# Performance work log

Hardware: AMD Instinct MI355X
Metric: run time of the kernel (lower is better)

Reference implementation:

```python
import jax, jax.numpy as jnp
import numpy as np

N_NODES = 100000
SELF_LOOP_W = 2.0  # improved=True in GCNConv -> A + 2I


def gcn_conv(x, src, dst, ew, W, b):
    """PyG GCNConv(improved=True): D^-1/2 (A + 2I) D^-1/2 X W + b.

    src/dst: edge endpoints, messages flow src -> dst (source_to_target).
    """
    n = x.shape[0]
    # degree after adding self loops with weight 2.0
    deg = jnp.zeros((n,), dtype=x.dtype).at[dst].add(ew) + SELF_LOOP_W
    dinv = jax.lax.rsqrt(deg)
    norm = dinv[src] * ew * dinv[dst]                      # [E]
    h = x @ W                                              # [N, out]
    agg = jax.ops.segment_sum(norm[:, None] * h[src], dst, num_segments=n)
    self_term = (SELF_LOOP_W * dinv * dinv)[:, None] * h   # self-loop edges
    return agg + self_term + b


def setup_inputs() -> dict:
    key = jax.random.key(0)
    ks = jax.random.split(key, 10)
    F_IN, H1, H2, C = 128, 128, 64, 5
    E = 1600000
    x = jax.random.normal(ks[0], (N_NODES, F_IN), dtype=jnp.float32)
    edge_index = jax.random.randint(ks[1], (2, E), 0, N_NODES, dtype=jnp.int64)
    edge_weight = jax.random.uniform(ks[2], (E,), dtype=jnp.float32)

    def glorot(k, shape):
        lim = float(np.sqrt(6.0 / (shape[0] + shape[1])))
        return jax.random.uniform(k, shape, jnp.float32, -lim, lim)

    return {
        "x": x,
        "edge_index": edge_index,
        "edge_weight": edge_weight,
        "W1": glorot(ks[3], (F_IN, H1)), "b1": jnp.zeros((H1,), jnp.float32),
        "W2": glorot(ks[4], (H1, H2)),  "b2": jnp.zeros((H2,), jnp.float32),
        "Wc": glorot(ks[5], (H2, C)),   "bc": jnp.zeros((C,), jnp.float32),
    }


def reference(x, edge_index, edge_weight, W1, b1, W2, b2, Wc, bc):
    src, dst = edge_index[0], edge_index[1]
    # conv1 + relu (dropout is identity in eval mode)
    h = jax.nn.relu(gcn_conv(x, src, dst, edge_weight, W1, b1))
    # conv2 + relu
    h = jax.nn.relu(gcn_conv(h, src, dst, edge_weight, W2, b2))
    # classifier head + log_softmax over classes
    logits = gcn_conv(h, src, dst, edge_weight, Wc, bc)
    return jax.nn.log_softmax(logits, axis=1)
```

## Files before the change

### kernel.cpp

```cpp
#include <hip/hip_runtime.h>
#include <hip/hip_bf16.h>

constexpr int TPB = 256;

static inline int cdiv(long long a, long long b) { return (int)((a + b - 1) / b); }

typedef __attribute__((ext_vector_type(8))) short bf16x8;
typedef __attribute__((ext_vector_type(4))) float f32x4;

__device__ inline unsigned short f2bf(float f) {
    __hip_bfloat16 h = __float2bfloat16(f);
    unsigned short u;
    __builtin_memcpy(&u, &h, 2);
    return u;
}

__device__ inline float bflo(unsigned u) { return __uint_as_float(u << 16); }
__device__ inline float bfhi(unsigned u) { return __uint_as_float(u & 0xffff0000u); }

__device__ inline unsigned relu_pk(unsigned w) {
    unsigned lo = (w & 0x8000u) ? 0u : (w & 0xFFFFu);
    unsigned hi = (w & 0x80000000u) ? 0u : (w & 0xFFFF0000u);
    return lo | hi;
}

constexpr int P1_CH   = 4096;
constexpr int MAXBINS = 512;
constexpr int BINCAP  = 4608;

__device__ __forceinline__ void part_body(const int* __restrict__ src,
                                          const int* __restrict__ dst,
                                          const float* __restrict__ ew,
                                          int* __restrict__ bincnt,
                                          int2* __restrict__ pbuf, int E, int nbins,
                                          int* h, int bid) {
    for (int t = threadIdx.x; t < nbins; t += TPB) h[t] = 0;
    __syncthreads();
    const int lo = bid * P1_CH;
    const int hi = min(lo + P1_CH, E);
    for (int e = lo + threadIdx.x; e < hi; e += TPB)
        atomicAdd(&h[dst[e] >> 8], 1);
    __syncthreads();
    for (int t = threadIdx.x; t < nbins; t += TPB) {
        int c = h[t];
        h[t] = (c > 0) ? atomicAdd(&bincnt[t], c) : 0;
    }
    __syncthreads();
    for (int e = lo + threadIdx.x; e < hi; e += TPB) {
        int d = dst[e];
        int bin = d >> 8;
        int idx = atomicAdd(&h[bin], 1);
        if (idx < BINCAP)
            pbuf[(size_t)bin * BINCAP + idx] =
                make_int2((src[e] & 0x1FFFF) | ((d & 255) << 24), __float_as_int(ew[e]));
    }
}

template<int CAP>
__global__ __launch_bounds__(TPB) void k_bucket(const int2* __restrict__ pbuf,
                                                const int* __restrict__ bincnt,
                                                int2* __restrict__ pairs,
                                                int* __restrict__ cnt,
                                                float* __restrict__ dinv, int n) {
    __shared__ int   lcnt[TPB];
    __shared__ float ldeg[TPB];
    const int tid = threadIdx.x;
    lcnt[tid] = 0; ldeg[tid] = 0.f;
    __syncthreads();
    const int bin = blockIdx.x;
    const int m = min(bincnt[bin], BINCAP);
    const int2* pb = pbuf + (size_t)bin * BINCAP;
    for (int i = tid; i < m; i += TPB) {
        int2 pe = pb[i];
        int dlo = (pe.x >> 24) & 255;
        int s   = pe.x & 0x1FFFF;
        int pos = atomicAdd(&lcnt[dlo], 1);
        if (pos < CAP)
            pairs[(size_t)(bin * 256 + dlo) * CAP + pos] = make_int2(s, pe.y);
        atomicAdd(&ldeg[dlo], __int_as_float(pe.y));
    }
    __syncthreads();
    int node = bin * 256 + tid;
    if (node < n) {
        cnt[node]  = min(lcnt[tid], CAP);
        dinv[node] = rsqrtf(ldeg[tid] + 2.0f);
    }
}

template<int CAP>
__global__ void k_bucket_scatter(const int* __restrict__ src, const int* __restrict__ dst,
                                 const float* __restrict__ ew, int* __restrict__ cnt,
                                 int2* __restrict__ pairs, int E) {
    int e = blockIdx.x * TPB + threadIdx.x;
    if (e >= E) return;
    int d = dst[e];
    int pos = atomicAdd(&cnt[d], 1);
    if (pos < CAP)
        pairs[(size_t)d * CAP + pos] = make_int2(src[e], __float_as_int(ew[e]));
}

template<int CAP>
__global__ void k_deg(const int2* __restrict__ pairs, const int* __restrict__ cnt,
                      float* __restrict__ dinv, int n) {
    int node = blockIdx.x * (TPB / 64) + (threadIdx.x >> 6);
    if (node >= n) return;
    int lane = threadIdx.x & 63;
    int m = min(cnt[node], CAP);
    float v = 0.f;
    if (lane < m) v = __int_as_float(pairs[(size_t)node * CAP + lane].y);
#pragma unroll
    for (int d = 1; d < 64; d <<= 1) v += __shfl_xor(v, d);
    if (lane == 0) dinv[node] = rsqrtf(v + 2.0f);
}

template<int CAP>
__global__ void k_normw(int2* __restrict__ pairs, const int* __restrict__ cnt,
                        const float* __restrict__ dinv, int n) {
    int lane = threadIdx.x & 63;
    int g = lane >> 4, o = lane & 15;
    int wid = blockIdx.x * (TPB / 64) + (threadIdx.x >> 6);
    int node = wid * 4 + g;
    if (node >= n) return;
    int m = min(cnt[node], CAP);
    float dd = dinv[node];
    int2* pr = pairs + (size_t)node * CAP;
    for (int j = o; j < m; j += 16) {
        int2 p = pr[j];
        pr[j].y = __float_as_int(dinv[p.x] * __int_as_float(p.y) * dd);
    }
}

__global__ void k_prepw(const float* __restrict__ W1, const float* __restrict__ W2,
                        __hip_bfloat16* __restrict__ Wt1, __hip_bfloat16* __restrict__ Wt2) {
    int i = blockIdx.x * TPB + threadIdx.x;
    if (i < 128 * 128) {
        int k = i >> 7, c = i & 127;
        Wt1[c * 128 + k] = __float2bfloat16(W1[i]);
    }
    if (i < 128 * 64) {
        int k = i >> 6, c = i & 63;
        Wt2[c * 128 + k] = __float2bfloat16(W2[i]);
    }
}


template<int KIN, int NCOL, bool RELU_IN, bool BF_IN>
__device__ __forceinline__ void gemm_mfma_body(const void* __restrict__ Xv,
                                               const __hip_bfloat16* __restrict__ Wt,
                                               __hip_bfloat16* __restrict__ H, int n,
                                               int bid, short* Xs) {
    constexpr int BM  = 128;
    constexpr int SX  = KIN + 8;
    constexpr int KCH = KIN / 32;
    constexpr int MT  = 4;
    constexpr int NT  = NCOL / 32;

    const int row0 = bid * BM;
    const int nrow = min(BM, n - row0);

    if constexpr (BF_IN) {
        const uint4* xg = (const uint4*)((const __hip_bfloat16*)Xv + (size_t)row0 * KIN);
        for (int i = threadIdx.x; i < BM * KIN / 8; i += TPB) {
            int r = i / (KIN / 8), c8 = i % (KIN / 8);
            uint4 v = make_uint4(0u, 0u, 0u, 0u);
            if (r < nrow) v = xg[i];
            if (RELU_IN) {
                v.x = relu_pk(v.x); v.y = relu_pk(v.y);
                v.z = relu_pk(v.z); v.w = relu_pk(v.w);
            }
            *(uint4*)&Xs[r * SX + c8 * 8] = v;
        }
    } else {
        const float4* xg = (const float4*)((const float*)Xv + (size_t)row0 * KIN);
        for (int i = threadIdx.x; i < BM * KIN / 4; i += TPB) {
            int r = i / (KIN / 4), c4 = i % (KIN / 4);
            float4 v = make_float4(0.f, 0.f, 0.f, 0.f);
            if (r < nrow) v = xg[i];
            if (RELU_IN) {
                v.x = fmaxf(v.x, 0.f); v.y = fmaxf(v.y, 0.f);
                v.z = fmaxf(v.z, 0.f); v.w = fmaxf(v.w, 0.f);
            }
            ushort4 b;
            b.x = f2bf(v.x); b.y = f2bf(v.y);
            b.z = f2bf(v.z); b.w = f2bf(v.w);
            *(ushort4*)&Xs[r * SX + c4 * 4] = b;
        }
    }
    __syncthreads();

    const int wave = threadIdx.x >> 6;
    const int lane = threadIdx.x & 63;
    const int wr = wave >> 1;
    const int wc = wave & 1;
    const int fr = lane & 15;
    const int fg = lane >> 4;

    f32x4 acc[MT][NT];
#pragma unroll
    for (int i = 0; i < MT; ++i)
#pragma unroll
        for (int j = 0; j < NT; ++j) acc[i][j] = (f32x4){0.f, 0.f, 0.f, 0.f};

    const short* xa = Xs + (wr * 64 + fr) * SX + fg * 8;
    const __hip_bfloat16* wg = Wt + (size_t)(wc * NT * 16 + fr) * KIN + fg * 8;

    bf16x8 bcur[NT], bnxt[NT];
#pragma unroll
    for (int j = 0; j < NT; ++j)
        bcur[j] = *(const bf16x8*)(wg + (size_t)j * 16 * KIN);

#pragma unroll
    for (int kc = 0; kc < KCH; ++kc) {
        bf16x8 a[MT];
#pragma unroll
        for (int i = 0; i < MT; ++i)
            a[i] = *(const bf16x8*)(xa + i * 16 * SX + kc * 32);
        if (kc + 1 < KCH) {
#pragma unroll
            for (int j = 0; j < NT; ++j)
                bnxt[j] = *(const bf16x8*)(wg + (size_t)j * 16 * KIN + (kc + 1) * 32);
        }
#pragma unroll
        for (int i = 0; i < MT; ++i)
#pragma unroll
            for (int j = 0; j < NT; ++j)
                acc[i][j] = __builtin_amdgcn_mfma_f32_16x16x32_bf16(a[i], bcur[j], acc[i][j], 0, 0, 0);
        if (kc + 1 < KCH) {
#pragma unroll
            for (int j = 0; j < NT; ++j) bcur[j] = bnxt[j];
        }
    }

#pragma unroll
    for (int i = 0; i < MT; ++i) {
#pragma unroll
        for (int j = 0; j < NT; ++j) {
            int col = wc * NT * 16 + j * 16 + fr;
            int rb  = wr * 64 + i * 16 + fg * 4;
#pragma unroll
            for (int q = 0; q < 4; ++q) {
                int r = rb + q;
                if (r < nrow)
                    H[(size_t)(row0 + r) * NCOL + col] = __float2bfloat16(acc[i][j][q]);
            }
        }
    }
}

template<int KIN, int NCOL, bool RELU_IN, bool BF_IN>
__global__ __launch_bounds__(TPB, 4) void k_gemm_mfma(const void* __restrict__ Xv,
                                                      const __hip_bfloat16* __restrict__ Wt,
                                                      __hip_bfloat16* __restrict__ H, int n) {
    __shared__ __align__(16) short Xs[128 * (KIN + 8)];
    gemm_mfma_body<KIN, NCOL, RELU_IN, BF_IN>(Xv, Wt, H, n, blockIdx.x, Xs);
}

__global__ __launch_bounds__(TPB, 4) void k_gemm1_part(
        const float* __restrict__ X, const __hip_bfloat16* __restrict__ Wt1,
        __hip_bfloat16* __restrict__ H, int n,
        const int* __restrict__ src, const int* __restrict__ dst,
        const float* __restrict__ ew, int* __restrict__ bincnt,
        int2* __restrict__ pbuf, int E, int nbins, int Gg, int Gp) {
    __shared__ __align__(16) short smem[128 * 136];
    int b = blockIdx.x;
    int r3 = b % 3;
    if (r3 == 2) {
        int pid = b / 3;
        if (pid < Gp) part_body(src, dst, ew, bincnt, pbuf, E, nbins, (int*)smem, pid);
    } else {
        int gid = (b / 3) * 2 + r3;
        if (gid < Gg) gemm_mfma_body<128, 128, false, false>(X, Wt1, H, n, gid, smem);
    }
}

template<int KIN, int KOUT, int OSTR, bool RELU_IN>
__global__ void k_gemv(const float* __restrict__ X, const float* __restrict__ W,
                       float* __restrict__ H, int n) {
    __shared__ float ws_[KIN * KOUT];
    for (int i = threadIdx.x; i < KIN * KOUT; i += TPB) ws_[i] = W[i];
    __syncthreads();
    int r = blockIdx.x * TPB + threadIdx.x;
    if (r >= n) return;
    float acc[KOUT];
#pragma unroll
    for (int c = 0; c < KOUT; ++c) acc[c] = 0.f;
    const float4* xr = (const float4*)(X + (size_t)r * KIN);
#pragma unroll
    for (int k4 = 0; k4 < KIN / 4; ++k4) {
        float4 xv = xr[k4];
        if (RELU_IN) {
            xv.x = fmaxf(xv.x, 0.f); xv.y = fmaxf(xv.y, 0.f);
            xv.z = fmaxf(xv.z, 0.f); xv.w = fmaxf(xv.w, 0.f);
        }
        float xs[4] = {xv.x, xv.y, xv.z, xv.w};
#pragma unroll
        for (int j = 0; j < 4; ++j)
#pragma unroll
            for (int c = 0; c < KOUT; ++c)
                acc[c] = fmaf(xs[j], ws_[(k4 * 4 + j) * KOUT + c], acc[c]);
    }
#pragma unroll
    for (int c = 0; c < KOUT; ++c) H[(size_t)r * OSTR + c] = acc[c];
#pragma unroll
    for (int c = KOUT; c < OSTR; ++c) H[(size_t)r * OSTR + c] = 0.f;
}


template<int K, int CAP, bool OUT_BF16>
__global__ __launch_bounds__(TPB) void k_agg_bf(const __hip_bfloat16* __restrict__ H,
                                                const int2* __restrict__ pairs,
                                                const int* __restrict__ cnt,
                                                const float* __restrict__ dinv,
                                                const float* __restrict__ b,
                                                void* __restrict__ out, int n) {
    constexpr int LPN = K / 8;
    constexpr int GPN = 64 / LPN;
    constexpr int RQ  = K / 8;
    constexpr int NCH = CAP / 8;
    const int lane = threadIdx.x & 63;
    const int g    = lane / LPN;
    const int o    = lane % LPN;
    const int wid  = blockIdx.x * (TPB / 64) + (threadIdx.x >> 6);
    const int node = wid * GPN + g;
    const bool alive = node < n;
    const int nc = alive ? node : 0;

    const uint4* __restrict__ Hq = (const uint4*)H;

    float di   = dinv[nc];
    float coef = 2.f * di * di;
    uint4 hv = Hq[(size_t)nc * RQ + o];
    const float4* bq = (const float4*)b + o * 2;
    float4 bA = bq[0], bB = bq[1];
    float acc[8];
    acc[0] = fmaf(coef, bflo(hv.x), bA.x);
    acc[1] = fmaf(coef, bfhi(hv.x), bA.y);
    acc[2] = fmaf(coef, bflo(hv.y), bA.z);
    acc[3] = fmaf(coef, bfhi(hv.y), bA.w);
    acc[4] = fmaf(coef, bflo(hv.z), bB.x);
    acc[5] = fmaf(coef, bfhi(hv.z), bB.y);
    acc[6] = fmaf(coef, bflo(hv.w), bB.z);
    acc[7] = fmaf(coef, bfhi(hv.w), bB.w);

    const int m = alive ? min(cnt[nc], CAP) : 0;
    const int2* pp = pairs + (size_t)nc * CAP;

    uint4 Ma[4], Mb[4];
#pragma unroll
    for (int q = 0; q < 4; ++q) Ma[q] = *(const uint4*)(pp + q * 2);

    auto chunk = [&](const uint4 (&Mc)[4], uint4 (&Mn)[4], int c) {
        const int base = c * 8;
        int s[8]; float w[8];
#pragma unroll
        for (int q = 0; q < 4; ++q) {
            s[2 * q]     = (int)Mc[q].x;  w[2 * q]     = __uint_as_float(Mc[q].y);
            s[2 * q + 1] = (int)Mc[q].z;  w[2 * q + 1] = __uint_as_float(Mc[q].w);
        }
        uint4 r[8];
#pragma unroll
        for (int u = 0; u < 8; ++u) {
            bool ok = (base + u) < m;
            int ss = ok ? s[u] : 0;
            if (!ok) w[u] = 0.f;
            r[u] = Hq[(size_t)ss * RQ + o];
        }
        if (base + 8 < m) {
#pragma unroll
            for (int q = 0; q < 4; ++q) Mn[q] = *(const uint4*)(pp + base + 8 + q * 2);
        }
#pragma unroll
        for (int u = 0; u < 8; ++u) {
            acc[0] = fmaf(w[u], bflo(r[u].x), acc[0]);
            acc[1] = fmaf(w[u], bfhi(r[u].x), acc[1]);
            acc[2] = fmaf(w[u], bflo(r[u].y), acc[2]);
            acc[3] = fmaf(w[u], bfhi(r[u].y), acc[3]);
            acc[4] = fmaf(w[u], bflo(r[u].z), acc[4]);
            acc[5] = fmaf(w[u], bfhi(r[u].z), acc[5]);
            acc[6] = fmaf(w[u], bflo(r[u].w), acc[6]);
            acc[7] = fmaf(w[u], bfhi(r[u].w), acc[7]);
        }
    };

#pragma unroll
    for (int c = 0; c < NCH; c += 2) {
        if (c * 8 >= m) break;
        chunk(Ma, Mb, c);
        if ((c + 1) * 8 >= m) break;
        chunk(Mb, Ma, c + 1);
    }

    if (alive) {
        if constexpr (OUT_BF16) {
            unsigned p0 = (unsigned)f2bf(acc[0]) | ((unsigned)f2bf(acc[1]) << 16);
            unsigned p1 = (unsigned)f2bf(acc[2]) | ((unsigned)f2bf(acc[3]) << 16);
            unsigned p2 = (unsigned)f2bf(acc[4]) | ((unsigned)f2bf(acc[5]) << 16);
            unsigned p3 = (unsigned)f2bf(acc[6]) | ((unsigned)f2bf(acc[7]) << 16);
            ((uint4*)out)[(size_t)node * RQ + o] = make_uint4(p0, p1, p2, p3);
        } else {
            float4* ap = (float4*)out + (size_t)node * (K / 4) + o * 2;
            ap[0] = make_float4(acc[0], acc[1], acc[2], acc[3]);
            ap[1] = make_float4(acc[4], acc[5], acc[6], acc[7]);
        }
    }
}

template<int CAP>
__global__ void k_agg5_lsm(const float* __restrict__ H, const int2* __restrict__ pairs,
                           const int* __restrict__ cnt, const float* __restrict__ dinv,
                           const float* __restrict__ b, float* __restrict__ out, int n) {
    constexpr int NCH = CAP / 8;
    int i = blockIdx.x * TPB + threadIdx.x;
    const bool alive = i < n;
    const int nc = alive ? i : 0;
    float di = dinv[nc];
    float coef = 2.f * di * di;
    float acc[5];
    {
        const float4 h0 = *(const float4*)(H + (size_t)nc * 8);
        const float  h4 = H[(size_t)nc * 8 + 4];
        acc[0] = fmaf(coef, h0.x, b[0]);
        acc[1] = fmaf(coef, h0.y, b[1]);
        acc[2] = fmaf(coef, h0.z, b[2]);
        acc[3] = fmaf(coef, h0.w, b[3]);
        acc[4] = fmaf(coef, h4,   b[4]);
    }
    const int m = alive ? min(cnt[nc], CAP) : 0;
    const int2* pp = pairs + (size_t)nc * CAP;

    uint4 Ma[4], Mb[4];
#pragma unroll
    for (int q = 0; q < 4; ++q) Ma[q] = *(const uint4*)(pp + q * 2);

    auto chunk = [&](const uint4 (&Mc)[4], uint4 (&Mn)[4], int c) {
        const int base = c * 8;
        int s[8]; float w[8];
#pragma unroll
        for (int q = 0; q < 4; ++q) {
            s[2 * q]     = (int)Mc[q].x;  w[2 * q]     = __uint_as_float(Mc[q].y);
            s[2 * q + 1] = (int)Mc[q].z;  w[2 * q + 1] = __uint_as_float(Mc[q].w);
        }
        float4 q0[8]; float q4[8];
#pragma unroll
        for (int u = 0; u < 8; ++u) {
            bool ok = (base + u) < m;
            int ss = ok ? s[u] : 0;
            if (!ok) w[u] = 0.f;
            const float* h = H + (size_t)ss * 8;
            q0[u] = *(const float4*)h;
            q4[u] = h[4];
        }
        if (base + 8 < m) {
#pragma unroll
            for (int q = 0; q < 4; ++q) Mn[q] = *(const uint4*)(pp + base + 8 + q * 2);
        }
#pragma unroll
        for (int u = 0; u < 8; ++u) {
            acc[0] = fmaf(w[u], q0[u].x, acc[0]);
            acc[1] = fmaf(w[u], q0[u].y, acc[1]);
            acc[2] = fmaf(w[u], q0[u].z, acc[2]);
            acc[3] = fmaf(w[u], q0[u].w, acc[3]);
            acc[4] = fmaf(w[u], q4[u],   acc[4]);
        }
    };

#pragma unroll
    for (int c = 0; c < NCH; c += 2) {
        if (c * 8 >= m) break;
        chunk(Ma, Mb, c);
        if ((c + 1) * 8 >= m) break;
        chunk(Mb, Ma, c + 1);
    }

    if (alive) {
        float mx = acc[0];
#pragma unroll
        for (int c = 1; c < 5; ++c) mx = fmaxf(mx, acc[c]);
        float ssum = 0.f;
#pragma unroll
        for (int c = 0; c < 5; ++c) ssum += expf(acc[c] - mx);
        float lg = mx + logf(ssum);
#pragma unroll
        for (int c = 0; c < 5; ++c) out[(size_t)i * 5 + c] = acc[c] - lg;
    }
}


template<int CAP>
static void run_all(const float* x, const int* srcv, const int* dstv, const float* ew,
                    const float* W1, const float* b1, const float* W2, const float* b2,
                    const float* Wc, const float* bc, float* out,
                    int n, int E, char* p, hipStream_t stream) {
    auto alloc = [&](size_t bytes) {
        char* r = p;
        p += (bytes + 255) & ~(size_t)255;
        return r;
    };
    float*          dinv   = (float*)alloc((size_t)n * 4);
    int*            cnt    = (int*)alloc((size_t)n * 4);
    int2*           pairs  = (int2*)alloc((size_t)n * CAP * 8);
    __hip_bfloat16* Hbf    = (__hip_bfloat16*)alloc((size_t)n * 128 * 2);
    __hip_bfloat16* A1bf   = (__hip_bfloat16*)alloc((size_t)n * 128 * 2);
    float*          bufB   = (float*)alloc((size_t)n * 64 * 4);
    float*          H3     = (float*)alloc((size_t)n * 8 * 4);
    int*            bincnt = (int*)alloc((size_t)MAXBINS * 4);
    int2*           pbuf   = (int2*)alloc((size_t)MAXBINS * BINCAP * 8);
    __hip_bfloat16* Wt1    = (__hip_bfloat16*)alloc(128 * 128 * 2);
    __hip_bfloat16* Wt2    = (__hip_bfloat16*)alloc(128 * 64 * 2);

    const int WPB = TPB / 64;
    const int nbins = cdiv(n, 256);

    k_prepw<<<cdiv(128 * 128, TPB), TPB, 0, stream>>>(W1, W2, Wt1, Wt2);

    if (nbins <= MAXBINS) {
        (void)hipMemsetAsync(bincnt, 0, (size_t)nbins * 4, stream);
        int Gg = cdiv(n, 128);
        int Gp = cdiv(E, P1_CH);
        int Gh = cdiv(Gg, 2);
        int G  = 3 * (Gp > Gh ? Gp : Gh);
        k_gemm1_part<<<G, TPB, 0, stream>>>(x, Wt1, Hbf, n, srcv, dstv, ew,
                                            bincnt, pbuf, E, nbins, Gg, Gp);
        k_bucket<CAP><<<nbins, TPB, 0, stream>>>(pbuf, bincnt, pairs, cnt, dinv, n);
    } else {
        (void)hipMemsetAsync(cnt, 0, (size_t)n * 4, stream);
        k_bucket_scatter<CAP><<<cdiv(E, TPB), TPB, 0, stream>>>(srcv, dstv, ew, cnt, pairs, E);
        k_deg<CAP><<<cdiv(n, WPB), TPB, 0, stream>>>(pairs, cnt, dinv, n);
        k_gemm_mfma<128, 128, false, false><<<cdiv(n, 128), TPB, 0, stream>>>(x, Wt1, Hbf, n);
    }
    k_normw<CAP><<<cdiv(n, WPB * 4), TPB, 0, stream>>>(pairs, cnt, dinv, n);

    k_agg_bf<128, CAP, true><<<cdiv(n, WPB * 4), TPB, 0, stream>>>(Hbf, pairs, cnt, dinv, b1, A1bf, n);

    k_gemm_mfma<128, 64, true, true><<<cdiv(n, 128), TPB, 0, stream>>>(A1bf, Wt2, Hbf, n);
    k_agg_bf<64, CAP, false><<<cdiv(n, WPB * 8), TPB, 0, stream>>>(Hbf, pairs, cnt, dinv, b2, bufB, n);

    k_gemv<64, 5, 8, true><<<cdiv(n, TPB), TPB, 0, stream>>>(bufB, Wc, H3, n);
    k_agg5_lsm<CAP><<<cdiv(n, TPB), TPB, 0, stream>>>(H3, pairs, cnt, dinv, bc, out, n);
}

extern "C" void kernel_launch(void* const* d_in, const int* in_sizes, int n_in,
                              void* d_out, int out_size, void* d_ws, size_t ws_size,
                              hipStream_t stream) {
    const float* x  = (const float*)d_in[0];
    const int*   ei = (const int*)d_in[1];
    const float* ew = (const float*)d_in[2];
    const float* W1 = (const float*)d_in[3];
    const float* b1 = (const float*)d_in[4];
    const float* W2 = (const float*)d_in[5];
    const float* b2 = (const float*)d_in[6];
    const float* Wc = (const float*)d_in[7];
    const float* bc = (const float*)d_in[8];

    const int E   = in_sizes[2];
    const int H1  = in_sizes[4];
    const int FIN = in_sizes[3] / H1;
    const int n   = in_sizes[0] / FIN;

    const int* srcv = ei;
    const int* dstv = ei + E;

    size_t fixed = ((size_t)n * 4 + 256) * 2 + ((size_t)n * 128 * 2 + 256) * 2 +
                   (size_t)n * 64 * 4 + 256 + (size_t)n * 8 * 4 + 256 +
                   (size_t)MAXBINS * 4 + 256 + (size_t)MAXBINS * BINCAP * 8 + 256 +
                   128 * 128 * 2 + 256 + 128 * 64 * 2 + 256 + 1024;
    if (ws_size == 0 || ws_size >= fixed + (size_t)n * 64 * 8)
        run_all<64>(x, srcv, dstv, ew, W1, b1, W2, b2, Wc, bc, (float*)d_out, n, E,
                    (char*)d_ws, stream);
    else
        run_all<48>(x, srcv, dstv, ew, W1, b1, W2, b2, Wc, bc, (float*)d_out, n, E,
                    (char*)d_ws, stream);
}
```

Measured before the change: 216.2 us.

## Replace binned two-pass CSR build with direct atomic scatter fused into GEMM1

Drops the bin-partition pass and the k_bucket kernel. Edges are now scattered straight into per-node slots using global atomics on counts, and degrees are accumulated with float atomics. A small kernel then turns degrees into dinv. This removes one kernel launch and the round trip through the intermediate partition buffer, but puts contended global atomics and uncoalesced writes on the scatter path, and makes degree summation order nondeterministic.

```diff
diff --git a/kernel.cpp b/kernel.cpp
--- a/kernel.cpp
+++ b/kernel.cpp
@@ -24,93 +24,31 @@
     return lo | hi;
 }
 
-constexpr int P1_CH   = 4096;
-constexpr int MAXBINS = 512;
-constexpr int BINCAP  = 4608;
-
-__device__ __forceinline__ void part_body(const int* __restrict__ src,
+constexpr int P1_CH = 4096;
+
+template<int CAP>
+__device__ __forceinline__ void scat_body(const int* __restrict__ src,
                                           const int* __restrict__ dst,
                                           const float* __restrict__ ew,
-                                          int* __restrict__ bincnt,
-                                          int2* __restrict__ pbuf, int E, int nbins,
-                                          int* h, int bid) {
-    for (int t = threadIdx.x; t < nbins; t += TPB) h[t] = 0;
-    __syncthreads();
+                                          int* __restrict__ cnt,
+                                          float* __restrict__ deg,
+                                          int2* __restrict__ pairs, int E, int bid) {
     const int lo = bid * P1_CH;
     const int hi = min(lo + P1_CH, E);
-    for (int e = lo + threadIdx.x; e < hi; e += TPB)
-        atomicAdd(&h[dst[e] >> 8], 1);
-    __syncthreads();
-    for (int t = threadIdx.x; t < nbins; t += TPB) {
-        int c = h[t];
-        h[t] = (c > 0) ? atomicAdd(&bincnt[t], c) : 0;
-    }
-    __syncthreads();
     for (int e = lo + threadIdx.x; e < hi; e += TPB) {
-        int d = dst[e];
-        int bin = d >> 8;
-        int idx = atomicAdd(&h[bin], 1);
-        if (idx < BINCAP)
-            pbuf[(size_t)bin * BINCAP + idx] =
-                make_int2((src[e] & 0x1FFFF) | ((d & 255) << 24), __float_as_int(ew[e]));
-    }
-}
-
-template<int CAP>
-__global__ __launch_bounds__(TPB) void k_bucket(const int2* __restrict__ pbuf,
-                                                const int* __restrict__ bincnt,
-                                                int2* __restrict__ pairs,
-                                                int* __restrict__ cnt,
-                                                float* __restrict__ dinv, int n) {
-    __shared__ int   lcnt[TPB];
-    __shared__ float ldeg[TPB];
-    const int tid = threadIdx.x;
-    lcnt[tid] = 0; ldeg[tid] = 0.f;
-    __syncthreads();
-    const int bin = blockIdx.x;
-    const int m = min(bincnt[bin], BINCAP);
-    const int2* pb = pbuf + (size_t)bin * BINCAP;
-    for (int i = tid; i < m; i += TPB) {
-        int2 pe = pb[i];
-        int dlo = (pe.x >> 24) & 255;
-        int s   = pe.x & 0x1FFFF;
-        int pos = atomicAdd(&lcnt[dlo], 1);
+        int d   = dst[e];
+        int s   = src[e];
+        float w = ew[e];
+        int pos = atomicAdd(&cnt[d], 1);
         if (pos < CAP)
-            pairs[(size_t)(bin * 256 + dlo) * CAP + pos] = make_int2(s, pe.y);
-        atomicAdd(&ldeg[dlo], __int_as_float(pe.y));
-    }
-    __syncthreads();
-    int node = bin * 256 + tid;
-    if (node < n) {
-        cnt[node]  = min(lcnt[tid], CAP);
-        dinv[node] = rsqrtf(ldeg[tid] + 2.0f);
-    }
-}
-
-template<int CAP>
-__global__ void k_bucket_scatter(const int* __restrict__ src, const int* __restrict__ dst,
-                                 const float* __restrict__ ew, int* __restrict__ cnt,
-                                 int2* __restrict__ pairs, int E) {
-    int e = blockIdx.x * TPB + threadIdx.x;
-    if (e >= E) return;
-    int d = dst[e];
-    int pos = atomicAdd(&cnt[d], 1);
-    if (pos < CAP)
-        pairs[(size_t)d * CAP + pos] = make_int2(src[e], __float_as_int(ew[e]));
-}
-
-template<int CAP>
-__global__ void k_deg(const int2* __restrict__ pairs, const int* __restrict__ cnt,
-                      float* __restrict__ dinv, int n) {
-    int node = blockIdx.x * (TPB / 64) + (threadIdx.x >> 6);
-    if (node >= n) return;
-    int lane = threadIdx.x & 63;
-    int m = min(cnt[node], CAP);
-    float v = 0.f;
-    if (lane < m) v = __int_as_float(pairs[(size_t)node * CAP + lane].y);
-#pragma unroll
-    for (int d = 1; d < 64; d <<= 1) v += __shfl_xor(v, d);
-    if (lane == 0) dinv[node] = rsqrtf(v + 2.0f);
+            pairs[(size_t)d * CAP + pos] = make_int2(s, __float_as_int(w));
+        atomicAdd(&deg[d], w);
+    }
+}
+
+__global__ void k_dinv(const float* __restrict__ deg, float* __restrict__ dinv, int n) {
+    int i = blockIdx.x * TPB + threadIdx.x;
+    if (i < n) dinv[i] = rsqrtf(deg[i] + 2.0f);
 }
 
 template<int CAP>
@@ -255,18 +193,20 @@
     gemm_mfma_body<KIN, NCOL, RELU_IN, BF_IN>(Xv, Wt, H, n, blockIdx.x, Xs);
 }
 
-__global__ __launch_bounds__(TPB, 4) void k_gemm1_part(
+template<int CAP>
+__global__ __launch_bounds__(TPB, 4) void k_gemm1_scat(
         const float* __restrict__ X, const __hip_bfloat16* __restrict__ Wt1,
         __hip_bfloat16* __restrict__ H, int n,
         const int* __restrict__ src, const int* __restrict__ dst,
-        const float* __restrict__ ew, int* __restrict__ bincnt,
-        int2* __restrict__ pbuf, int E, int nbins, int Gg, int Gp) {
+        const float* __restrict__ ew, int* __restrict__ cnt,
+        float* __restrict__ deg, int2* __restrict__ pairs,
+        int E, int Gg, int Gp) {
     __shared__ __align__(16) short smem[128 * 136];
     int b = blockIdx.x;
     int r3 = b % 3;
     if (r3 == 2) {
         int pid = b / 3;
-        if (pid < Gp) part_body(src, dst, ew, bincnt, pbuf, E, nbins, (int*)smem, pid);
+        if (pid < Gp) scat_body<CAP>(src, dst, ew, cnt, deg, pairs, E, pid);
     } else {
         int gid = (b / 3) * 2 + r3;
         if (gid < Gg) gemm_mfma_body<128, 128, false, false>(X, Wt1, H, n, gid, smem);
@@ -498,36 +438,30 @@
     };
     float*          dinv   = (float*)alloc((size_t)n * 4);
     int*            cnt    = (int*)alloc((size_t)n * 4);
+    float*          deg    = (float*)alloc((size_t)n * 4);
     int2*           pairs  = (int2*)alloc((size_t)n * CAP * 8);
     __hip_bfloat16* Hbf    = (__hip_bfloat16*)alloc((size_t)n * 128 * 2);
     __hip_bfloat16* A1bf   = (__hip_bfloat16*)alloc((size_t)n * 128 * 2);
     float*          bufB   = (float*)alloc((size_t)n * 64 * 4);
     float*          H3     = (float*)alloc((size_t)n * 8 * 4);
-    int*            bincnt = (int*)alloc((size_t)MAXBINS * 4);
-    int2*           pbuf   = (int2*)alloc((size_t)MAXBINS * BINCAP * 8);
     __hip_bfloat16* Wt1    = (__hip_bfloat16*)alloc(128 * 128 * 2);
     __hip_bfloat16* Wt2    = (__hip_bfloat16*)alloc(128 * 64 * 2);
 
     const int WPB = TPB / 64;
-    const int nbins = cdiv(n, 256);
 
     k_prepw<<<cdiv(128 * 128, TPB), TPB, 0, stream>>>(W1, W2, Wt1, Wt2);
-
-    if (nbins <= MAXBINS) {
-        (void)hipMemsetAsync(bincnt, 0, (size_t)nbins * 4, stream);
+    (void)hipMemsetAsync(cnt, 0, (size_t)n * 4, stream);
+    (void)hipMemsetAsync(deg, 0, (size_t)n * 4, stream);
+
+    {
         int Gg = cdiv(n, 128);
         int Gp = cdiv(E, P1_CH);
         int Gh = cdiv(Gg, 2);
         int G  = 3 * (Gp > Gh ? Gp : Gh);
-        k_gemm1_part<<<G, TPB, 0, stream>>>(x, Wt1, Hbf, n, srcv, dstv, ew,
-                                            bincnt, pbuf, E, nbins, Gg, Gp);
-        k_bucket<CAP><<<nbins, TPB, 0, stream>>>(pbuf, bincnt, pairs, cnt, dinv, n);
-    } else {
-        (void)hipMemsetAsync(cnt, 0, (size_t)n * 4, stream);
-        k_bucket_scatter<CAP><<<cdiv(E, TPB), TPB, 0, stream>>>(srcv, dstv, ew, cnt, pairs, E);
-        k_deg<CAP><<<cdiv(n, WPB), TPB, 0, stream>>>(pairs, cnt, dinv, n);
-        k_gemm_mfma<128, 128, false, false><<<cdiv(n, 128), TPB, 0, stream>>>(x, Wt1, Hbf, n);
-    }
+        k_gemm1_scat<CAP><<<G, TPB, 0, stream>>>(x, Wt1, Hbf, n, srcv, dstv, ew,
+                                                 cnt, deg, pairs, E, Gg, Gp);
+    }
+    k_dinv<<<cdiv(n, TPB), TPB, 0, stream>>>(deg, dinv, n);
     k_normw<CAP><<<cdiv(n, WPB * 4), TPB, 0, stream>>>(pairs, cnt, dinv, n);
 
     k_agg_bf<128, CAP, true><<<cdiv(n, WPB * 4), TPB, 0, stream>>>(Hbf, pairs, cnt, dinv, b1, A1bf, n);
@@ -560,9 +494,8 @@
     const int* srcv = ei;
     const int* dstv = ei + E;
 
-    size_t fixed = ((size_t)n * 4 + 256) * 2 + ((size_t)n * 128 * 2 + 256) * 2 +
+    size_t fixed = ((size_t)n * 4 + 256) * 3 + ((size_t)n * 128 * 2 + 256) * 2 +
                    (size_t)n * 64 * 4 + 256 + (size_t)n * 8 * 4 + 256 +
-                   (size_t)MAXBINS * 4 + 256 + (size_t)MAXBINS * BINCAP * 8 + 256 +
                    128 * 128 * 2 + 256 + 128 * 64 * 2 + 256 + 1024;
     if (ws_size == 0 || ws_size >= fixed + (size_t)n * 64 * 8)
         run_all<64>(x, srcv, dstv, ew, W1, b1, W2, b2, Wc, bc, (float*)d_out, n, E,
```

New measurement: 311.7 us. +44.2%, slower.

## Fuse layer-1 aggregation into layer-2 GEMM and layer-2 aggregation into classifier GEMV

Applied to the files above, without the earlier changes.

The layer-1 neighbor aggregation now writes its ReLU'd bf16 rows straight into LDS, and the same block runs the MFMA GEMM with W2 on them. This removes the A1bf intermediate round trip through global memory and one kernel launch. Layer-2 aggregation likewise applies ReLU and the 64x5 classifier projection in registers, reduced with a cross-lane shuffle. That removes the fp32 bufB write/read and the separate GEMV launch. The trade-off is that the fused aggregation kernel has 128 rows per block with heavy LDS use, which lowers occupancy for the latency-bound gather phase.

```diff
diff --git a/kernel.cpp b/kernel.cpp
--- a/kernel.cpp
+++ b/kernel.cpp
@@ -144,17 +144,83 @@
 }
 
 
+template<int KIN, int NCOL>
+__device__ __forceinline__ void gemm_from_lds(const short* Xs,
+                                              const __hip_bfloat16* __restrict__ Wt,
+                                              __hip_bfloat16* __restrict__ H,
+                                              int n, int row0) {
+    constexpr int SX  = KIN + 8;
+    constexpr int KCH = KIN / 32;
+    constexpr int MT  = 4;
+    constexpr int NT  = NCOL / 32;
+    const int nrow = min(128, n - row0);
+
+    const int wave = threadIdx.x >> 6;
+    const int lane = threadIdx.x & 63;
+    const int wr = wave >> 1;
+    const int wc = wave & 1;
+    const int fr = lane & 15;
+    const int fg = lane >> 4;
+
+    f32x4 acc[MT][NT];
+#pragma unroll
+    for (int i = 0; i < MT; ++i)
+#pragma unroll
+        for (int j = 0; j < NT; ++j) acc[i][j] = (f32x4){0.f, 0.f, 0.f, 0.f};
+
+    const short* xa = Xs + (wr * 64 + fr) * SX + fg * 8;
+    const __hip_bfloat16* wg = Wt + (size_t)(wc * NT * 16 + fr) * KIN + fg * 8;
+
+    bf16x8 bcur[NT], bnxt[NT];
+#pragma unroll
+    for (int j = 0; j < NT; ++j)
+        bcur[j] = *(const bf16x8*)(wg + (size_t)j * 16 * KIN);
+
+#pragma unroll
+    for (int kc = 0; kc < KCH; ++kc) {
+        bf16x8 a[MT];
+#pragma unroll
+        for (int i = 0; i < MT; ++i)
+            a[i] = *(const bf16x8*)(xa + i * 16 * SX + kc * 32);
+        if (kc + 1 < KCH) {
+#pragma unroll
+            for (int j = 0; j < NT; ++j)
+                bnxt[j] = *(const bf16x8*)(wg + (size_t)j * 16 * KIN + (kc + 1) * 32);
+        }
+#pragma unroll
+        for (int i = 0; i < MT; ++i)
+#pragma unroll
+            for (int j = 0; j < NT; ++j)
+                acc[i][j] = __builtin_amdgcn_mfma_f32_16x16x32_bf16(a[i], bcur[j], acc[i][j], 0, 0, 0);
+        if (kc + 1 < KCH) {
+#pragma unroll
+            for (int j = 0; j < NT; ++j) bcur[j] = bnxt[j];
+        }
+    }
+
+#pragma unroll
+    for (int i = 0; i < MT; ++i) {
+#pragma unroll
+        for (int j = 0; j < NT; ++j) {
+            int col = wc * NT * 16 + j * 16 + fr;
+            int rb  = wr * 64 + i * 16 + fg * 4;
+#pragma unroll
+            for (int q = 0; q < 4; ++q) {
+                int r = rb + q;
+                if (r < nrow)
+                    H[(size_t)(row0 + r) * NCOL + col] = __float2bfloat16(acc[i][j][q]);
+            }
+        }
+    }
+}
+
 template<int KIN, int NCOL, bool RELU_IN, bool BF_IN>
 __device__ __forceinline__ void gemm_mfma_body(const void* __restrict__ Xv,
                                                const __hip_bfloat16* __restrict__ Wt,
                                                __hip_bfloat16* __restrict__ H, int n,
                                                int bid, short* Xs) {
-    constexpr int BM  = 128;
-    constexpr int SX  = KIN + 8;
-    constexpr int KCH = KIN / 32;
-    constexpr int MT  = 4;
-    constexpr int NT  = NCOL / 32;
-
+    constexpr int BM = 128;
+    constexpr int SX = KIN + 8;
     const int row0 = bid * BM;
     const int nrow = min(BM, n - row0);
 
@@ -187,64 +253,7 @@
         }
     }
     __syncthreads();
-
-    const int wave = threadIdx.x >> 6;
-    const int lane = threadIdx.x & 63;
-    const int wr = wave >> 1;
-    const int wc = wave & 1;
-    const int fr = lane & 15;
-    const int fg = lane >> 4;
-
-    f32x4 acc[MT][NT];
-#pragma unroll
-    for (int i = 0; i < MT; ++i)
-#pragma unroll
-        for (int j = 0; j < NT; ++j) acc[i][j] = (f32x4){0.f, 0.f, 0.f, 0.f};
-
-    const short* xa = Xs + (wr * 64 + fr) * SX + fg * 8;
-    const __hip_bfloat16* wg = Wt + (size_t)(wc * NT * 16 + fr) * KIN + fg * 8;
-
-    bf16x8 bcur[NT], bnxt[NT];
-#pragma unroll
-    for (int j = 0; j < NT; ++j)
-        bcur[j] = *(const bf16x8*)(wg + (size_t)j * 16 * KIN);
-
-#pragma unroll
-    for (int kc = 0; kc < KCH; ++kc) {
-        bf16x8 a[MT];
-#pragma unroll
-        for (int i = 0; i < MT; ++i)
-            a[i] = *(const bf16x8*)(xa + i * 16 * SX + kc * 32);
-        if (kc + 1 < KCH) {
-#pragma unroll
-            for (int j = 0; j < NT; ++j)
-                bnxt[j] = *(const bf16x8*)(wg + (size_t)j * 16 * KIN + (kc + 1) * 32);
-        }
-#pragma unroll
-        for (int i = 0; i < MT; ++i)
-#pragma unroll
-            for (int j = 0; j < NT; ++j)
-                acc[i][j] = __builtin_amdgcn_mfma_f32_16x16x32_bf16(a[i], bcur[j], acc[i][j], 0, 0, 0);
-        if (kc + 1 < KCH) {
-#pragma unroll
-            for (int j = 0; j < NT; ++j) bcur[j] = bnxt[j];
-        }
-    }
-
-#pragma unroll
-    for (int i = 0; i < MT; ++i) {
-#pragma unroll
-        for (int j = 0; j < NT; ++j) {
-            int col = wc * NT * 16 + j * 16 + fr;
-            int rb  = wr * 64 + i * 16 + fg * 4;
-#pragma unroll
-            for (int q = 0; q < 4; ++q) {
-                int r = rb + q;
-                if (r < nrow)
-                    H[(size_t)(row0 + r) * NCOL + col] = __float2bfloat16(acc[i][j][q]);
-            }
-        }
-    }
+    gemm_from_lds<KIN, NCOL>(Xs, Wt, H, n, row0);
 }
 
 template<int KIN, int NCOL, bool RELU_IN, bool BF_IN>
@@ -273,59 +282,128 @@
     }
 }
 
-template<int KIN, int KOUT, int OSTR, bool RELU_IN>
-__global__ void k_gemv(const float* __restrict__ X, const float* __restrict__ W,
-                       float* __restrict__ H, int n) {
-    __shared__ float ws_[KIN * KOUT];
-    for (int i = threadIdx.x; i < KIN * KOUT; i += TPB) ws_[i] = W[i];
-    __syncthreads();
-    int r = blockIdx.x * TPB + threadIdx.x;
-    if (r >= n) return;
-    float acc[KOUT];
-#pragma unroll
-    for (int c = 0; c < KOUT; ++c) acc[c] = 0.f;
-    const float4* xr = (const float4*)(X + (size_t)r * KIN);
-#pragma unroll
-    for (int k4 = 0; k4 < KIN / 4; ++k4) {
-        float4 xv = xr[k4];
-        if (RELU_IN) {
-            xv.x = fmaxf(xv.x, 0.f); xv.y = fmaxf(xv.y, 0.f);
-            xv.z = fmaxf(xv.z, 0.f); xv.w = fmaxf(xv.w, 0.f);
-        }
-        float xs[4] = {xv.x, xv.y, xv.z, xv.w};
-#pragma unroll
-        for (int j = 0; j < 4; ++j)
-#pragma unroll
-            for (int c = 0; c < KOUT; ++c)
-                acc[c] = fmaf(xs[j], ws_[(k4 * 4 + j) * KOUT + c], acc[c]);
-    }
-#pragma unroll
-    for (int c = 0; c < KOUT; ++c) H[(size_t)r * OSTR + c] = acc[c];
-#pragma unroll
-    for (int c = KOUT; c < OSTR; ++c) H[(size_t)r * OSTR + c] = 0.f;
-}
-
-
-template<int K, int CAP, bool OUT_BF16>
-__global__ __launch_bounds__(TPB) void k_agg_bf(const __hip_bfloat16* __restrict__ H,
-                                                const int2* __restrict__ pairs,
-                                                const int* __restrict__ cnt,
-                                                const float* __restrict__ dinv,
-                                                const float* __restrict__ b,
-                                                void* __restrict__ out, int n) {
-    constexpr int LPN = K / 8;
-    constexpr int GPN = 64 / LPN;
-    constexpr int RQ  = K / 8;
+
+template<int CAP>
+__global__ __launch_bounds__(TPB, 4) void k_agg1_gemm2(
+        const __hip_bfloat16* __restrict__ H, const int2* __restrict__ pairs,
+        const int* __restrict__ cnt, const float* __restrict__ dinv,
+        const float* __restrict__ b, const __hip_bfloat16* __restrict__ Wt2,
+        __hip_bfloat16* __restrict__ H2, int n) {
+    constexpr int RQ  = 16;
     constexpr int NCH = CAP / 8;
+    constexpr int SX  = 136;
+    __shared__ __align__(16) short Xs[128 * SX];
+
     const int lane = threadIdx.x & 63;
-    const int g    = lane / LPN;
-    const int o    = lane % LPN;
-    const int wid  = blockIdx.x * (TPB / 64) + (threadIdx.x >> 6);
-    const int node = wid * GPN + g;
+    const int wave = threadIdx.x >> 6;
+    const int g = lane >> 4;
+    const int o = lane & 15;
+    const int row0 = blockIdx.x * 128;
+
+    const uint4* __restrict__ Hq = (const uint4*)H;
+    const float4* bq = (const float4*)b + o * 2;
+    const float4 bA = bq[0], bB = bq[1];
+
+    for (int it = 0; it < 8; ++it) {
+        const int rloc = wave * 32 + it * 4 + g;
+        const int node = row0 + rloc;
+        const bool alive = node < n;
+        const int nc = alive ? node : 0;
+
+        float di   = dinv[nc];
+        float coef = 2.f * di * di;
+        uint4 hv = Hq[(size_t)nc * RQ + o];
+        float acc[8];
+        acc[0] = fmaf(coef, bflo(hv.x), bA.x);
+        acc[1] = fmaf(coef, bfhi(hv.x), bA.y);
+        acc[2] = fmaf(coef, bflo(hv.y), bA.z);
+        acc[3] = fmaf(coef, bfhi(hv.y), bA.w);
+        acc[4] = fmaf(coef, bflo(hv.z), bB.x);
+        acc[5] = fmaf(coef, bfhi(hv.z), bB.y);
+        acc[6] = fmaf(coef, bflo(hv.w), bB.z);
+        acc[7] = fmaf(coef, bfhi(hv.w), bB.w);
+
+        const int m = alive ? min(cnt[nc], CAP) : 0;
+        const int2* pp = pairs + (size_t)nc * CAP;
+
+        uint4 Ma[4], Mb[4];
+#pragma unroll
+        for (int q = 0; q < 4; ++q) Ma[q] = *(const uint4*)(pp + q * 2);
+
+        auto chunk = [&](const uint4 (&Mc)[4], uint4 (&Mn)[4], int c) {
+            const int base = c * 8;
+            int s[8]; float w[8];
+#pragma unroll
+            for (int q = 0; q < 4; ++q) {
+                s[2 * q]     = (int)Mc[q].x;  w[2 * q]     = __uint_as_float(Mc[q].y);
+                s[2 * q + 1] = (int)Mc[q].z;  w[2 * q + 1] = __uint_as_float(Mc[q].w);
+            }
+            uint4 r[8];
+#pragma unroll
+            for (int u = 0; u < 8; ++u) {
+                bool ok = (base + u) < m;
+                int ss = ok ? s[u] : 0;
+                if (!ok) w[u] = 0.f;
+                r[u] = Hq[(size_t)ss * RQ + o];
+            }
+            if (base + 8 < m) {
+#pragma unroll
+                for (int q = 0; q < 4; ++q) Mn[q] = *(const uint4*)(pp + base + 8 + q * 2);
+            }
+#pragma unroll
+            for (int u = 0; u < 8; ++u) {
+                acc[0] = fmaf(w[u], bflo(r[u].x), acc[0]);
+                acc[1] = fmaf(w[u], bfhi(r[u].x), acc[1]);
+                acc[2] = fmaf(w[u], bflo(r[u].y), acc[2]);
+                acc[3] = fmaf(w[u], bfhi(r[u].y), acc[3]);
+                acc[4] = fmaf(w[u], bflo(r[u].z), acc[4]);
+                acc[5] = fmaf(w[u], bfhi(r[u].z), acc[5]);
+                acc[6] = fmaf(w[u], bflo(r[u].w), acc[6]);
+                acc[7] = fmaf(w[u], bfhi(r[u].w), acc[7]);
+            }
+        };
+
+#pragma unroll
+        for (int c = 0; c < NCH; c += 2) {
+            if (c * 8 >= m) break;
+            chunk(Ma, Mb, c);
+            if ((c + 1) * 8 >= m) break;
+            chunk(Mb, Ma, c + 1);
+        }
+
+        unsigned p0 = (unsigned)f2bf(acc[0]) | ((unsigned)f2bf(acc[1]) << 16);
+        unsigned p1 = (unsigned)f2bf(acc[2]) | ((unsigned)f2bf(acc[3]) << 16);
+        unsigned p2 = (unsigned)f2bf(acc[4]) | ((unsigned)f2bf(acc[5]) << 16);
+        unsigned p3 = (unsigned)f2bf(acc[6]) | ((unsigned)f2bf(acc[7]) << 16);
+        *(uint4*)&Xs[rloc * SX + o * 8] =
+            make_uint4(relu_pk(p0), relu_pk(p1), relu_pk(p2), relu_pk(p3));
+    }
+    __syncthreads();
+    gemm_from_lds<128, 64>(Xs, Wt2, H2, n, row0);
+}
+
+
+template<int CAP>
+__global__ __launch_bounds__(TPB) void k_agg2_gemv(
+        const __hip_bfloat16* __restrict__ H2, const int2* __restrict__ pairs,
+        const int* __restrict__ cnt, const float* __restrict__ dinv,
+        const float* __restrict__ b, const float* __restrict__ Wc,
+        float* __restrict__ H3, int n) {
+    constexpr int RQ  = 8;
+    constexpr int NCH = CAP / 8;
+    __shared__ float ws_[64 * 5];
+    for (int i = threadIdx.x; i < 64 * 5; i += TPB) ws_[i] = Wc[i];
+    __syncthreads();
+
+    const int lane = threadIdx.x & 63;
+    const int g = lane >> 3;
+    const int o = lane & 7;
+    const int wid = blockIdx.x * (TPB / 64) + (threadIdx.x >> 6);
+    const int node = wid * 8 + g;
     const bool alive = node < n;
     const int nc = alive ? node : 0;
 
-    const uint4* __restrict__ Hq = (const uint4*)H;
+    const uint4* __restrict__ Hq = (const uint4*)H2;
 
     float di   = dinv[nc];
     float coef = 2.f * di * di;
@@ -390,18 +468,22 @@
         chunk(Mb, Ma, c + 1);
     }
 
-    if (alive) {
-        if constexpr (OUT_BF16) {
-            unsigned p0 = (unsigned)f2bf(acc[0]) | ((unsigned)f2bf(acc[1]) << 16);
-            unsigned p1 = (unsigned)f2bf(acc[2]) | ((unsigned)f2bf(acc[3]) << 16);
-            unsigned p2 = (unsigned)f2bf(acc[4]) | ((unsigned)f2bf(acc[5]) << 16);
-            unsigned p3 = (unsigned)f2bf(acc[6]) | ((unsigned)f2bf(acc[7]) << 16);
-            ((uint4*)out)[(size_t)node * RQ + o] = make_uint4(p0, p1, p2, p3);
-        } else {
-            float4* ap = (float4*)out + (size_t)node * (K / 4) + o * 2;
-            ap[0] = make_float4(acc[0], acc[1], acc[2], acc[3]);
-            ap[1] = make_float4(acc[4], acc[5], acc[6], acc[7]);
-        }
+    float p[5] = {0.f, 0.f, 0.f, 0.f, 0.f};
+#pragma unroll
+    for (int j = 0; j < 8; ++j) {
+        float h = fmaxf(acc[j], 0.f);
+        const float* wr_ = ws_ + (o * 8 + j) * 5;
+#pragma unroll
+        for (int c = 0; c < 5; ++c) p[c] = fmaf(h, wr_[c], p[c]);
+    }
+#pragma unroll
+    for (int d = 1; d < 8; d <<= 1)
+#pragma unroll
+        for (int c = 0; c < 5; ++c) p[c] += __shfl_xor(p[c], d);
+    if (alive && o == 0) {
+        float* hp = H3 + (size_t)node * 8;
+#pragma unroll
+        for (int c = 0; c < 5; ++c) hp[c] = p[c];
     }
 }
 
@@ -500,8 +582,7 @@
     int*            cnt    = (int*)alloc((size_t)n * 4);
     int2*           pairs  = (int2*)alloc((size_t)n * CAP * 8);
     __hip_bfloat16* Hbf    = (__hip_bfloat16*)alloc((size_t)n * 128 * 2);
-    __hip_bfloat16* A1bf   = (__hip_bfloat16*)alloc((size_t)n * 128 * 2);
-    float*          bufB   = (float*)alloc((size_t)n * 64 * 4);
+    __hip_bfloat16* H2     = (__hip_bfloat16*)alloc((size_t)n * 64 * 2);
     float*          H3     = (float*)alloc((size_t)n * 8 * 4);
     int*            bincnt = (int*)alloc((size_t)MAXBINS * 4);
     int2*           pbuf   = (int2*)alloc((size_t)MAXBINS * BINCAP * 8);
@@ -530,12 +611,10 @@
     }
     k_normw<CAP><<<cdiv(n, WPB * 4), TPB, 0, stream>>>(pairs, cnt, dinv, n);
 
-    k_agg_bf<128, CAP, true><<<cdiv(n, WPB * 4), TPB, 0, stream>>>(Hbf, pairs, cnt, dinv, b1, A1bf, n);
-
-    k_gemm_mfma<128, 64, true, true><<<cdiv(n, 128), TPB, 0, stream>>>(A1bf, Wt2, Hbf, n);
-    k_agg_bf<64, CAP, false><<<cdiv(n, WPB * 8), TPB, 0, stream>>>(Hbf, pairs, cnt, dinv, b2, bufB, n);
-
-    k_gemv<64, 5, 8, true><<<cdiv(n, TPB), TPB, 0, stream>>>(bufB, Wc, H3, n);
+    k_agg1_gemm2<CAP><<<cdiv(n, 128), TPB, 0, stream>>>(Hbf, pairs, cnt, dinv, b1, Wt2, H2, n);
+
+    k_agg2_gemv<CAP><<<cdiv(n, WPB * 8), TPB, 0, stream>>>(H2, pairs, cnt, dinv, b2, Wc, H3, n);
+
     k_agg5_lsm<CAP><<<cdiv(n, TPB), TPB, 0, stream>>>(H3, pairs, cnt, dinv, bc, out, n);
 }
 
@@ -560,8 +639,8 @@
     const int* srcv = ei;
     const int* dstv = ei + E;
 
-    size_t fixed = ((size_t)n * 4 + 256) * 2 + ((size_t)n * 128 * 2 + 256) * 2 +
-                   (size_t)n * 64 * 4 + 256 + (size_t)n * 8 * 4 + 256 +
+    size_t fixed = ((size_t)n * 4 + 256) * 2 + (size_t)n * 128 * 2 + 256 +
+                   (size_t)n * 64 * 2 + 256 + (size_t)n * 8 * 4 + 256 +
                    (size_t)MAXBINS * 4 + 256 + (size_t)MAXBINS * BINCAP * 8 + 256 +
                    128 * 128 * 2 + 256 + 128 * 64 * 2 + 256 + 1024;
     if (ws_size == 0 || ws_size >= fixed + (size_t)n * 64 * 8)
```

Result: faster. 208.8 us (-3.4%).
